# Kernel tuning notes

Hardware: AMD Instinct MI355X
Metric: run time of the kernel (lower is better)

## Reference

```python
import jax, jax.numpy as jnp
import numpy as np

H = 256      # hidden_dim
NH = 4       # num_heads
DK = H // NH # per-head dim
NL = 2       # num self-attn layers
TL = 6       # transformer_num_layers (output repeat)
PTS_DIM = 3


def _layer_norm(x, g, b, eps=1e-5):
    m = jnp.mean(x, axis=-1, keepdims=True)
    v = jnp.mean((x - m) ** 2, axis=-1, keepdims=True)
    return (x - m) / jnp.sqrt(v + eps) * g + b


def _mha(x, Wq, bq, Wk, bk, Wv, bv, Wo, bo, g, bb, bias):
    # x: [B,N,H]; bias: [B,NH,N,N]; way='add' (att_spm_type='add')
    B, N, _ = x.shape
    q = (x @ Wq + bq).reshape(B, N, NH, DK).transpose(0, 2, 1, 3)  # [B,h,N,d]
    k = (x @ Wk + bk).reshape(B, N, NH, DK).transpose(0, 2, 1, 3)
    v = (x @ Wv + bv).reshape(B, N, NH, DK).transpose(0, 2, 1, 3)
    att = jnp.einsum('bhnd,bhmd->bhnm', q, k) / np.sqrt(DK).astype(np.float32)
    att = jax.nn.softmax(att + bias, axis=-1)
    out = jnp.einsum('bhnm,bhmd->bhnd', att, v).transpose(0, 2, 1, 3).reshape(B, N, H)
    out = out @ Wo + bo
    return _layer_norm(x + out, g, bb)


def setup_inputs() -> dict:
    key = jax.random.key(0)
    ks = jax.random.split(key, 16)
    B, N = 1, 512
    s = 0.02  # weight init scale
    inp = {
        'history_states': jax.random.normal(ks[0], (TL, B, N, H), jnp.float32),
        'all_lanes_preds': jax.random.normal(ks[1], (TL, B, N, 33), jnp.float32),
        'fc_W': jax.random.normal(ks[2], (H, H), jnp.float32) * s,
        'fc_b': jnp.zeros((H,), jnp.float32),
        'Wq': jax.random.normal(ks[3], (NL, H, H), jnp.float32) * s,
        'bq': jnp.zeros((NL, H), jnp.float32),
        'Wk': jax.random.normal(ks[4], (NL, H, H), jnp.float32) * s,
        'bk': jnp.zeros((NL, H), jnp.float32),
        'Wv': jax.random.normal(ks[5], (NL, H, H), jnp.float32) * s,
        'bv': jnp.zeros((NL, H), jnp.float32),
        'Wo': jax.random.normal(ks[6], (NL, H, H), jnp.float32) * s,
        'bo': jnp.zeros((NL, H), jnp.float32),
        'ln_g': jnp.ones((NL, H), jnp.float32),
        'ln_b': jnp.zeros((NL, H), jnp.float32),
        'mlp1_W': jax.random.normal(ks[7], (H, H), jnp.float32) * s,
        'mlp1_b': jnp.zeros((H,), jnp.float32),
        'mlp2_W': jax.random.normal(ks[8], (H, H), jnp.float32) * s,
        'mlp2_b': jnp.zeros((H,), jnp.float32),
        'cls_W1': jax.random.normal(ks[9], (2 * H, H), jnp.float32) * s,
        'cls_b1': jnp.zeros((H,), jnp.float32),
        'cls_W2': jax.random.normal(ks[10], (H, 1), jnp.float32) * s,
        'cls_b2': jnp.zeros((1,), jnp.float32),
    }
    return inp


def reference(history_states, all_lanes_preds, fc_W, fc_b, Wq, bq, Wk, bk, Wv, bv,
              Wo, bo, ln_g, ln_b, mlp1_W, mlp1_b, mlp2_W, mlp2_b,
              cls_W1, cls_b1, cls_W2, cls_b2):
    query_feats = history_states[-1]                 # [B,N,H]
    coords = all_lanes_preds[-1]                      # [B,N,33]
    B, N, C = coords.shape
    coords = coords.reshape(B, N, C // PTS_DIM, PTS_DIM)
    query_end_point = coords[:, :, -1, :]             # [B,N,3]
    key_start_point = coords[:, :, 0, :]              # [B,N,3]

    # pairwise distance bias: dist[b,i,j] = ||key_start[j] - query_end[i]||
    diff = key_start_point[:, None, :, :] - query_end_point[:, :, None, :]
    dist = jnp.sqrt(jnp.sum(diff ** 2, axis=-1))[:, None, :, :]  # [B,1,N,N]
    dw = 1.0 / (dist + 0.01)
    dw = dw / jnp.sum(dw, axis=2, keepdims=True)      # normalize over dim 2
    zeros = jnp.zeros_like(dw)
    dist_weights = jax.lax.stop_gradient(
        jnp.concatenate([dw, -dist, zeros, zeros], axis=1))  # [B,4,N,N]

    # features_concat: Linear + ReLU
    x = jax.nn.relu(query_feats @ fc_W + fc_b)

    for i in range(NL):
        x = _mha(x, Wq[i], bq[i], Wk[i], bk[i], Wv[i], bv[i],
                 Wo[i], bo[i], ln_g[i], ln_b[i], dist_weights)

    # lclc relationship head: per-side MLP, pairwise concat, classifier
    o1 = jax.nn.relu(x @ mlp1_W + mlp1_b)             # [B,N,H]
    o2 = jax.nn.relu(x @ mlp2_W + mlp2_b)
    pair = jnp.concatenate([
        jnp.broadcast_to(o1[:, :, None, :], (B, N, N, H)),
        jnp.broadcast_to(o2[:, None, :, :], (B, N, N, H))], axis=-1)  # [B,N,N,2H]
    z = jax.nn.relu(pair @ cls_W1 + cls_b1)
    lclc = (z @ cls_W2 + cls_b2)[..., 0]              # [B,N,N]
    all_lclc_preds = jnp.broadcast_to(lclc[None], (TL, B, N, N))
    return all_lclc_preds
```

## Files before the change

### kernel.cpp

```cpp
#include <hip/hip_runtime.h>
#include <math.h>


#define NTOK 512
#define HDIM 256
#define DKH  64
#define NHEAD 4
#define TLEN 6
#define WSZ  65536
#define PSTR 520
#define XPS  264

typedef __attribute__((ext_vector_type(8))) short bf16x8;
typedef __attribute__((ext_vector_type(4))) float f32x4;

__device__ __forceinline__ ushort f2bf(float f)
{
    unsigned u = __builtin_bit_cast(unsigned, f);
    u += 0x7FFFu + ((u >> 16) & 1u);
    return (ushort)(u >> 16);
}

struct PKArg {
    const float* w[13];
    const float* pl;
    ushort* wpk;
    float *dist, *dwraw, *inv_cs;
};

__global__ __launch_bounds__(256) void pack_kernel(PKArg p)
{
    __shared__ __align__(16) ushort smu[64 * 72];
    const int bid = blockIdx.x;
    const int t   = threadIdx.x;

    if (bid < 208) {
        const int mat  = bid >> 4;
        const int tile = bid & 15;
        const int k0   = (tile >> 2) * 64;
        const int c0   = (tile & 3) * 64;
        const float* W = p.w[mat];
#pragma unroll
        for (int j = 0; j < 4; ++j) {
            const int i  = t + j * 256;
            const int r  = i >> 4, c4 = i & 15;
            const float4 v4 = *(const float4*)&W[(k0 + r) * HDIM + c0 + c4 * 4];
            smu[(c4 * 4 + 0) * 72 + r] = f2bf(v4.x);
            smu[(c4 * 4 + 1) * 72 + r] = f2bf(v4.y);
            smu[(c4 * 4 + 2) * 72 + r] = f2bf(v4.z);
            smu[(c4 * 4 + 3) * 72 + r] = f2bf(v4.w);
        }
        __syncthreads();
#pragma unroll
        for (int j = 0; j < 2; ++j) {
            const int i  = t + j * 256;
            const int cr = i >> 3, kk = i & 7;
            const uint4 v = *(const uint4*)&smu[cr * 72 + kk * 8];
            *(uint4*)&p.wpk[mat * WSZ + (c0 + cr) * HDIM + k0 + kk * 8] = v;
        }
    } else {
        float* smf = (float*)smu;
        float* qe  = smf;
        float* red = smf + 1536;
        const int item = bid - 208;
        for (int i = t; i < 512; i += 256) {
            qe[i * 3 + 0] = p.pl[i * 33 + 30];
            qe[i * 3 + 1] = p.pl[i * 33 + 31];
            qe[i * 3 + 2] = p.pl[i * 33 + 32];
        }
        __syncthreads();
        const int m   = item * 64 + (t & 63);
        const int nch = t >> 6;
        const float kx = p.pl[m * 33 + 0], ky = p.pl[m * 33 + 1], kz = p.pl[m * 33 + 2];
        float cs = 0.f;
        for (int n = nch * 128; n < nch * 128 + 128; ++n) {
            const float dx = kx - qe[n * 3 + 0];
            const float dy = ky - qe[n * 3 + 1];
            const float dz = kz - qe[n * 3 + 2];
            const float dd = sqrtf(dx * dx + dy * dy + dz * dz);
            const float w  = 1.0f / (dd + 0.01f);
            p.dist[n * NTOK + m]  = dd;
            p.dwraw[n * NTOK + m] = w;
            cs += w;
        }
        red[nch * 64 + (t & 63)] = cs;
        __syncthreads();
        if (t < 64)
            p.inv_cs[item * 64 + t] =
                1.0f / (red[t] + red[64 + t] + red[128 + t] + red[192 + t]);
    }
}

__device__ __forceinline__ void qkv_one(
    const ushort* __restrict__ xpan, const ushort* __restrict__ Wt,
    const float* __restrict__ bb, int p,
    int slab, int c0, int lr, int lg, int lk,
    ushort* __restrict__ q16, ushort* __restrict__ k16,
    ushort* __restrict__ vT16)
{
    const ushort* Ap = xpan + lr * XPS + lk;
    f32x4 acc[4];
#pragma unroll
    for (int j = 0; j < 4; ++j) acc[j] = (f32x4){0.f, 0.f, 0.f, 0.f};
#pragma unroll
    for (int ks = 0; ks < 8; ++ks) {
        const bf16x8 a = *(const bf16x8*)&Ap[ks * 32];
#pragma unroll
        for (int j = 0; j < 4; ++j) {
            const bf16x8 b = *(const bf16x8*)&Wt[(c0 + j * 16 + lr) * HDIM + ks * 32 + lk];
            acc[j] = __builtin_amdgcn_mfma_f32_16x16x32_bf16(a, b, acc[j], 0, 0, 0);
        }
    }
#pragma unroll
    for (int j = 0; j < 4; ++j) {
        const int col = c0 + j * 16 + lr;
        const float bv2 = bb[col];
        if (p < 2) {
            ushort* dst = (p == 0) ? q16 : k16;
#pragma unroll
            for (int rg = 0; rg < 4; ++rg)
                dst[(slab + lg * 4 + rg) * HDIM + col] = f2bf(acc[j][rg] + bv2);
        } else {
            ushort4 s = {f2bf(acc[j][0] + bv2), f2bf(acc[j][1] + bv2),
                         f2bf(acc[j][2] + bv2), f2bf(acc[j][3] + bv2)};
            *(ushort4*)&vT16[col * NTOK + slab + lg * 4] = s;
        }
    }
}

__global__ __launch_bounds__(256) void fcqkv(
    const float* __restrict__ qf, const ushort* __restrict__ fcWt,
    const float* __restrict__ fcb,
    const ushort* __restrict__ WqT, const float* __restrict__ bq,
    const ushort* __restrict__ WkT, const float* __restrict__ bk,
    const ushort* __restrict__ WvT, const float* __restrict__ bv,
    float* __restrict__ x, ushort* __restrict__ q16,
    ushort* __restrict__ k16, ushort* __restrict__ vT16)
{
    __shared__ __align__(16) ushort xpan[16 * XPS];
    const int bid  = blockIdx.x;
    const int p    = bid >> 5;
    const int slab = (bid & 31) * 16;
    const int t = threadIdx.x;
    const int wv = t >> 6, lane = t & 63;
    const int lr = lane & 15, lg = lane >> 4, lk = lg * 8;
    const int c0 = wv * 64;

    {
        f32x4 acc[4];
#pragma unroll
        for (int j = 0; j < 4; ++j) acc[j] = (f32x4){0.f, 0.f, 0.f, 0.f};
        const float* Aq = qf + (slab + lr) * HDIM + lk;
#pragma unroll
        for (int ks = 0; ks < 8; ++ks) {
            const float4 a0 = *(const float4*)&Aq[ks * 32];
            const float4 a1 = *(const float4*)&Aq[ks * 32 + 4];
            bf16x8 a;
            a[0] = (short)f2bf(a0.x); a[1] = (short)f2bf(a0.y);
            a[2] = (short)f2bf(a0.z); a[3] = (short)f2bf(a0.w);
            a[4] = (short)f2bf(a1.x); a[5] = (short)f2bf(a1.y);
            a[6] = (short)f2bf(a1.z); a[7] = (short)f2bf(a1.w);
#pragma unroll
            for (int j = 0; j < 4; ++j) {
                const bf16x8 b = *(const bf16x8*)&fcWt[(c0 + j * 16 + lr) * HDIM + ks * 32 + lk];
                acc[j] = __builtin_amdgcn_mfma_f32_16x16x32_bf16(a, b, acc[j], 0, 0, 0);
            }
        }
#pragma unroll
        for (int j = 0; j < 4; ++j) {
            const int col = c0 + j * 16 + lr;
            const float bbv = fcb[col];
#pragma unroll
            for (int rg = 0; rg < 4; ++rg) {
                const float o = fmaxf(acc[j][rg] + bbv, 0.f);
                if (p == 0) x[(slab + lg * 4 + rg) * HDIM + col] = o;
                xpan[(lg * 4 + rg) * XPS + col] = f2bf(o);
            }
        }
    }
    __syncthreads();
    const ushort* Wt = (p == 0) ? WqT : (p == 1) ? WkT : WvT;
    const float*  bb = (p == 0) ? bq  : (p == 1) ? bk  : bv;
    qkv_one(xpan, Wt, bb, p, slab, c0, lr, lg, lk, q16, k16, vT16);
}

__global__ __launch_bounds__(256) void attn_fused(
    const ushort* __restrict__ q16, const ushort* __restrict__ k16,
    const ushort* __restrict__ vT16, const float* __restrict__ dist,
    const float* __restrict__ dwraw, const float* __restrict__ inv_cs,
    ushort* __restrict__ ao16)
{
    __shared__ __align__(16) ushort P_lds[16 * PSTR];
    __shared__ __align__(16) float exch[4][16][64];
    __shared__ float rmax[4][16];
    __shared__ float psums[4][16];

    const int bid = blockIdx.x;
    const int h  = bid >> 5;
    const int n0 = (bid & 31) * 16;
    const int t  = threadIdx.x;
    const int wv = t >> 6, lane = t & 63;
    const int lr = lane & 15, lg = lane >> 4, lk = lg * 8;
    const int mW = wv * 128;

    const ushort* Qrow = q16 + (n0 + lr) * HDIM + h * DKH + lk;
    const bf16x8 a0 = *(const bf16x8*)&Qrow[0];
    const bf16x8 a1 = *(const bf16x8*)&Qrow[32];

    f32x4 accs[8];
#pragma unroll
    for (int cg = 0; cg < 8; ++cg) accs[cg] = (f32x4){0.f, 0.f, 0.f, 0.f};
#pragma unroll
    for (int cg = 0; cg < 8; ++cg) {
        const ushort* Brow = k16 + (mW + cg * 16 + lr) * HDIM + h * DKH + lk;
        accs[cg] = __builtin_amdgcn_mfma_f32_16x16x32_bf16(
            a0, *(const bf16x8*)&Brow[0], accs[cg], 0, 0, 0);
        accs[cg] = __builtin_amdgcn_mfma_f32_16x16x32_bf16(
            a1, *(const bf16x8*)&Brow[32], accs[cg], 0, 0, 0);
    }

    float s[8][4];
#pragma unroll
    for (int cg = 0; cg < 8; ++cg) {
        const int m = mW + cg * 16 + lr;
        const float ic = (h == 0) ? inv_cs[m] : 0.f;
#pragma unroll
        for (int rg = 0; rg < 4; ++rg) {
            const int n = n0 + lg * 4 + rg;
            float b = 0.f;
            if (h == 0)      b = dwraw[n * NTOK + m] * ic;
            else if (h == 1) b = -dist[n * NTOK + m];
            s[cg][rg] = accs[cg][rg] * 0.125f + b;
        }
    }

    float mx[4];
#pragma unroll
    for (int rg = 0; rg < 4; ++rg) {
        float m = s[0][rg];
#pragma unroll
        for (int cg = 1; cg < 8; ++cg) m = fmaxf(m, s[cg][rg]);
#pragma unroll
        for (int o = 1; o < 16; o <<= 1) m = fmaxf(m, __shfl_xor(m, o));
        mx[rg] = m;
    }
    if (lr == 0)
#pragma unroll
        for (int rg = 0; rg < 4; ++rg) rmax[wv][lg * 4 + rg] = mx[rg];
    __syncthreads();
    float mxf[4];
#pragma unroll
    for (int rg = 0; rg < 4; ++rg) {
        const int row = lg * 4 + rg;
        mxf[rg] = fmaxf(fmaxf(rmax[0][row], rmax[1][row]),
                        fmaxf(rmax[2][row], rmax[3][row]));
    }

    float ps[4] = {0.f, 0.f, 0.f, 0.f};
#pragma unroll
    for (int cg = 0; cg < 8; ++cg)
#pragma unroll
        for (int rg = 0; rg < 4; ++rg) {
            const float e = __expf(s[cg][rg] - mxf[rg]);
            ps[rg] += e;
            P_lds[(lg * 4 + rg) * PSTR + mW + cg * 16 + lr] = f2bf(e);
        }
#pragma unroll
    for (int rg = 0; rg < 4; ++rg) {
#pragma unroll
        for (int o = 1; o < 16; o <<= 1) ps[rg] += __shfl_xor(ps[rg], o);
    }
    if (lr == 0)
#pragma unroll
        for (int rg = 0; rg < 4; ++rg) psums[wv][lg * 4 + rg] = ps[rg];
    __syncthreads();

    f32x4 acco[4];
#pragma unroll
    for (int db = 0; db < 4; ++db) acco[db] = (f32x4){0.f, 0.f, 0.f, 0.f};
#pragma unroll
    for (int c = 0; c < 4; ++c) {
        const bf16x8 pa = *(const bf16x8*)&P_lds[lr * PSTR + mW + c * 32 + lk];
#pragma unroll
        for (int db = 0; db < 4; ++db) {
            const bf16x8 b = *(const bf16x8*)
                &vT16[(h * DKH + db * 16 + lr) * NTOK + mW + c * 32 + lk];
            acco[db] = __builtin_amdgcn_mfma_f32_16x16x32_bf16(pa, b, acco[db], 0, 0, 0);
        }
    }
#pragma unroll
    for (int db = 0; db < 4; ++db)
#pragma unroll
        for (int rg = 0; rg < 4; ++rg)
            exch[wv][lg * 4 + rg][db * 16 + lr] = acco[db][rg];
    __syncthreads();

    {
        const int r = t >> 4, d4 = t & 15;
        f32x4 sum = *(const f32x4*)&exch[0][r][d4 * 4];
        sum += *(const f32x4*)&exch[1][r][d4 * 4];
        sum += *(const f32x4*)&exch[2][r][d4 * 4];
        sum += *(const f32x4*)&exch[3][r][d4 * 4];
        const float inv = 1.0f / (psums[0][r] + psums[1][r] + psums[2][r] + psums[3][r]);
        ushort4 o = {f2bf(sum.x * inv), f2bf(sum.y * inv),
                     f2bf(sum.z * inv), f2bf(sum.w * inv)};
        *(ushort4*)&ao16[(n0 + r) * HDIM + h * DKH + d4 * 4] = o;
    }
}

__device__ __forceinline__ void oprojln_phase(
    const ushort* __restrict__ ao16, const ushort* __restrict__ WoT,
    const float* __restrict__ bo, const float* __restrict__ gamma,
    const float* __restrict__ beta, const float* __restrict__ x,
    int slab, int c0, int wv, int lr, int lg, int lk,
    float red[4][16], f32x4 acc[4])
{
    const ushort* Arow = ao16 + (slab + lr) * HDIM + lk;
#pragma unroll
    for (int j = 0; j < 4; ++j) acc[j] = (f32x4){0.f, 0.f, 0.f, 0.f};
#pragma unroll
    for (int ks = 0; ks < 8; ++ks) {
        const bf16x8 a = *(const bf16x8*)&Arow[ks * 32];
#pragma unroll
        for (int j = 0; j < 4; ++j) {
            const bf16x8 b = *(const bf16x8*)&WoT[(c0 + j * 16 + lr) * HDIM + ks * 32 + lk];
            acc[j] = __builtin_amdgcn_mfma_f32_16x16x32_bf16(a, b, acc[j], 0, 0, 0);
        }
    }
#pragma unroll
    for (int j = 0; j < 4; ++j) {
        const int col = c0 + j * 16 + lr;
        const float bc = bo[col];
#pragma unroll
        for (int rg = 0; rg < 4; ++rg)
            acc[j][rg] += bc + x[(slab + lg * 4 + rg) * HDIM + col];
    }

    float sm[4];
#pragma unroll
    for (int rg = 0; rg < 4; ++rg) {
        float s = 0.f;
#pragma unroll
        for (int j = 0; j < 4; ++j) s += acc[j][rg];
#pragma unroll
        for (int o = 1; o < 16; o <<= 1) s += __shfl_xor(s, o);
        sm[rg] = s;
    }
    if (lr == 0)
#pragma unroll
        for (int rg = 0; rg < 4; ++rg) red[wv][lg * 4 + rg] = sm[rg];
    __syncthreads();
    float mean[4];
#pragma unroll
    for (int rg = 0; rg < 4; ++rg) {
        const int row = lg * 4 + rg;
        mean[rg] = (red[0][row] + red[1][row] + red[2][row] + red[3][row]) * (1.f / 256.f);
    }
    __syncthreads();

#pragma unroll
    for (int rg = 0; rg < 4; ++rg) {
        float s2 = 0.f;
#pragma unroll
        for (int j = 0; j < 4; ++j) {
            const float c = acc[j][rg] - mean[rg];
            s2 += c * c;
        }
#pragma unroll
        for (int o = 1; o < 16; o <<= 1) s2 += __shfl_xor(s2, o);
        sm[rg] = s2;
    }
    if (lr == 0)
#pragma unroll
        for (int rg = 0; rg < 4; ++rg) red[wv][lg * 4 + rg] = sm[rg];
    __syncthreads();
    float rstd[4];
#pragma unroll
    for (int rg = 0; rg < 4; ++rg) {
        const int row = lg * 4 + rg;
        const float var = (red[0][row] + red[1][row] + red[2][row] + red[3][row]) * (1.f / 256.f);
        rstd[rg] = rsqrtf(var + 1e-5f);
    }
#pragma unroll
    for (int j = 0; j < 4; ++j) {
        const int col = c0 + j * 16 + lr;
        const float gg = gamma[col], bv = beta[col];
#pragma unroll
        for (int rg = 0; rg < 4; ++rg)
            acc[j][rg] = (acc[j][rg] - mean[rg]) * rstd[rg] * gg + bv;
    }
}

__global__ __launch_bounds__(256) void oprojqkv(
    const ushort* __restrict__ ao16, const ushort* __restrict__ WoT,
    const float* __restrict__ bo, const float* __restrict__ gamma,
    const float* __restrict__ beta,
    const ushort* __restrict__ WqT, const float* __restrict__ bq,
    const ushort* __restrict__ WkT, const float* __restrict__ bk,
    const ushort* __restrict__ WvT, const float* __restrict__ bv,
    float* __restrict__ x, ushort* __restrict__ q16,
    ushort* __restrict__ k16, ushort* __restrict__ vT16)
{
    __shared__ __align__(16) ushort xpan[16 * XPS];
    __shared__ float red[4][16];
    const int bid  = blockIdx.x;
    const int p    = bid >> 5;
    const int slab = (bid & 31) * 16;
    const int t = threadIdx.x;
    const int wv = t >> 6, lane = t & 63;
    const int lr = lane & 15, lg = lane >> 4, lk = lg * 8;
    const int c0 = wv * 64;

    f32x4 acc[4];
    oprojln_phase(ao16, WoT, bo, gamma, beta, x, slab, c0, wv, lr, lg, lk, red, acc);
#pragma unroll
    for (int j = 0; j < 4; ++j) {
        const int col = c0 + j * 16 + lr;
#pragma unroll
        for (int rg = 0; rg < 4; ++rg) {
            if (p == 0) x[(slab + lg * 4 + rg) * HDIM + col] = acc[j][rg];
            xpan[(lg * 4 + rg) * XPS + col] = f2bf(acc[j][rg]);
        }
    }
    __syncthreads();
    const ushort* Wt = (p == 0) ? WqT : (p == 1) ? WkT : WvT;
    const float*  bb = (p == 0) ? bq  : (p == 1) ? bk  : bv;
    qkv_one(xpan, Wt, bb, p, slab, c0, lr, lg, lk, q16, k16, vT16);
}

__global__ __launch_bounds__(256) void oprojmlpU(
    const ushort* __restrict__ ao16, const ushort* __restrict__ WoT,
    const float* __restrict__ bo, const float* __restrict__ gamma,
    const float* __restrict__ beta,
    const ushort* __restrict__ m1WT, const float* __restrict__ m1b,
    const ushort* __restrict__ m2WT, const float* __restrict__ m2b,
    const ushort* __restrict__ cW1aT, const float* __restrict__ cb1,
    const ushort* __restrict__ cW1bT,
    const float* __restrict__ x, float* __restrict__ U1, float* __restrict__ U2)
{
    __shared__ __align__(16) ushort xpan[16 * XPS];
    __shared__ __align__(16) ushort opan[16 * XPS];
    __shared__ float red[4][16];
    const int bid  = blockIdx.x;
    const int p    = bid >> 5;
    const int slab = (bid & 31) * 16;
    const int t = threadIdx.x;
    const int wv = t >> 6, lane = t & 63;
    const int lr = lane & 15, lg = lane >> 4, lk = lg * 8;
    const int c0 = wv * 64;

    f32x4 acc[4];
    oprojln_phase(ao16, WoT, bo, gamma, beta, x, slab, c0, wv, lr, lg, lk, red, acc);
#pragma unroll
    for (int j = 0; j < 4; ++j) {
        const int col = c0 + j * 16 + lr;
#pragma unroll
        for (int rg = 0; rg < 4; ++rg)
            xpan[(lg * 4 + rg) * XPS + col] = f2bf(acc[j][rg]);
    }
    __syncthreads();

    {
        const ushort* Wt = p ? m2WT : m1WT;
        const float*  bb = p ? m2b  : m1b;
        const ushort* Ap = xpan + lr * XPS + lk;
        f32x4 a2[4];
#pragma unroll
        for (int j = 0; j < 4; ++j) a2[j] = (f32x4){0.f, 0.f, 0.f, 0.f};
#pragma unroll
        for (int ks = 0; ks < 8; ++ks) {
            const bf16x8 a = *(const bf16x8*)&Ap[ks * 32];
#pragma unroll
            for (int j = 0; j < 4; ++j) {
                const bf16x8 b = *(const bf16x8*)&Wt[(c0 + j * 16 + lr) * HDIM + ks * 32 + lk];
                a2[j] = __builtin_amdgcn_mfma_f32_16x16x32_bf16(a, b, a2[j], 0, 0, 0);
            }
        }
#pragma unroll
        for (int j = 0; j < 4; ++j) {
            const int col = c0 + j * 16 + lr;
            const float bbv = bb[col];
#pragma unroll
            for (int rg = 0; rg < 4; ++rg)
                opan[(lg * 4 + rg) * XPS + col] = f2bf(fmaxf(a2[j][rg] + bbv, 0.f));
        }
    }
    __syncthreads();

    {
        const ushort* Wt = p ? cW1bT : cW1aT;
        float* U         = p ? U2 : U1;
        const ushort* Ao = opan + lr * XPS + lk;
        f32x4 a2[4];
#pragma unroll
        for (int j = 0; j < 4; ++j) a2[j] = (f32x4){0.f, 0.f, 0.f, 0.f};
#pragma unroll
        for (int ks = 0; ks < 8; ++ks) {
            const bf16x8 a = *(const bf16x8*)&Ao[ks * 32];
#pragma unroll
            for (int j = 0; j < 4; ++j) {
                const bf16x8 b = *(const bf16x8*)&Wt[(c0 + j * 16 + lr) * HDIM + ks * 32 + lk];
                a2[j] = __builtin_amdgcn_mfma_f32_16x16x32_bf16(a, b, a2[j], 0, 0, 0);
            }
        }
#pragma unroll
        for (int j = 0; j < 4; ++j) {
            const int col = c0 + j * 16 + lr;
            const float bbv = (p == 0) ? cb1[col] : 0.f;
#pragma unroll
            for (int rg = 0; rg < 4; ++rg)
                U[(slab + lg * 4 + rg) * HDIM + col] = a2[j][rg] + bbv;
        }
    }
}

__global__ __launch_bounds__(256) void pair_cls(const float* __restrict__ U1,
                                                const float* __restrict__ U2,
                                                const float* __restrict__ W2,
                                                const float* __restrict__ b2,
                                                float* __restrict__ out)
{
    __shared__ __align__(16) float u1s[32][260];
    __shared__ __align__(16) float u2s[32][260];
    __shared__ __align__(16) float w2s[256];
    const int t  = threadIdx.x;
    const int n0 = blockIdx.y * 32, m0 = blockIdx.x * 32;

    for (int i = t; i < 32 * 64; i += 256) {
        const int r = i >> 6, c4 = i & 63;
        *(float4*)&u1s[r][c4 * 4] = *(const float4*)&U1[(n0 + r) * HDIM + c4 * 4];
        *(float4*)&u2s[r][c4 * 4] = *(const float4*)&U2[(m0 + r) * HDIM + c4 * 4];
    }
    if (t < 64) *(float4*)&w2s[t * 4] = *(const float4*)&W2[t * 4];
    __syncthreads();

    const int tx = t & 15, ty = t >> 4;
    float acc[2][2] = {};
    for (int h4 = 0; h4 < 64; ++h4) {
        const float4 a0 = *(const float4*)&u1s[ty * 2][h4 * 4];
        const float4 a1 = *(const float4*)&u1s[ty * 2 + 1][h4 * 4];
        const float4 b0 = *(const float4*)&u2s[tx * 2][h4 * 4];
        const float4 b1 = *(const float4*)&u2s[tx * 2 + 1][h4 * 4];
        const float4 w  = *(const float4*)&w2s[h4 * 4];
#define RT(A, B) fmaxf((A) + (B), 0.f)
        acc[0][0] += RT(a0.x,b0.x)*w.x + RT(a0.y,b0.y)*w.y + RT(a0.z,b0.z)*w.z + RT(a0.w,b0.w)*w.w;
        acc[0][1] += RT(a0.x,b1.x)*w.x + RT(a0.y,b1.y)*w.y + RT(a0.z,b1.z)*w.z + RT(a0.w,b1.w)*w.w;
        acc[1][0] += RT(a1.x,b0.x)*w.x + RT(a1.y,b0.y)*w.y + RT(a1.z,b0.z)*w.z + RT(a1.w,b0.w)*w.w;
        acc[1][1] += RT(a1.x,b1.x)*w.x + RT(a1.y,b1.y)*w.y + RT(a1.z,b1.z)*w.z + RT(a1.w,b1.w)*w.w;
#undef RT
    }
    const float bbv = b2[0];
#pragma unroll
    for (int ii = 0; ii < 2; ++ii)
#pragma unroll
        for (int jj = 0; jj < 2; ++jj) {
            const float val = acc[ii][jj] + bbv;
            const int n = n0 + ty * 2 + ii;
            const int m = m0 + tx * 2 + jj;
#pragma unroll
            for (int tl = 0; tl < TLEN; ++tl)
                out[tl * NTOK * NTOK + n * NTOK + m] = val;
        }
}

extern "C" void kernel_launch(void* const* d_in, const int* in_sizes, int n_in,
                              void* d_out, int out_size, void* d_ws, size_t ws_size,
                              hipStream_t stream)
{
    const float* hs   = (const float*)d_in[0];
    const float* qf   = hs + 5 * NTOK * HDIM;
    const float* alp  = (const float*)d_in[1];
    const float* pl   = alp + 5 * NTOK * 33;
    const float* fc_W = (const float*)d_in[2];
    const float* fc_b = (const float*)d_in[3];
    const float* Wq   = (const float*)d_in[4];
    const float* bq   = (const float*)d_in[5];
    const float* Wk   = (const float*)d_in[6];
    const float* bk   = (const float*)d_in[7];
    const float* Wv   = (const float*)d_in[8];
    const float* bv   = (const float*)d_in[9];
    const float* Wo   = (const float*)d_in[10];
    const float* bo   = (const float*)d_in[11];
    const float* lng  = (const float*)d_in[12];
    const float* lnb  = (const float*)d_in[13];
    const float* m1W  = (const float*)d_in[14];
    const float* m1b  = (const float*)d_in[15];
    const float* m2W  = (const float*)d_in[16];
    const float* m2b  = (const float*)d_in[17];
    const float* cW1  = (const float*)d_in[18];
    const float* cb1  = (const float*)d_in[19];
    const float* cW2  = (const float*)d_in[20];
    const float* cb2  = (const float*)d_in[21];
    float* out = (float*)d_out;

    const int NN  = NTOK * NTOK;
    const int NH_ = NTOK * HDIM;
    float* ws     = (float*)d_ws;
    float* dist   = ws;
    float* dwraw  = ws + NN;
    float* inv_cs = ws + 2 * NN;
    float* x      = ws + 2 * NN + 512;
    float* U1     = x + NH_;
    float* U2     = U1 + NH_;
    ushort* u16   = (ushort*)(U2 + NH_);
    ushort* wpk   = u16;
    ushort* q16   = wpk + 13 * WSZ;
    ushort* k16   = q16 + NH_;
    ushort* vT16  = k16 + NH_;
    ushort* ao16  = vT16 + NH_;

    PKArg pk;
    pk.w[0]  = fc_W;
    pk.w[1]  = Wq;  pk.w[2]  = Wq + WSZ;
    pk.w[3]  = Wk;  pk.w[4]  = Wk + WSZ;
    pk.w[5]  = Wv;  pk.w[6]  = Wv + WSZ;
    pk.w[7]  = Wo;  pk.w[8]  = Wo + WSZ;
    pk.w[9]  = m1W; pk.w[10] = m2W;
    pk.w[11] = cW1; pk.w[12] = cW1 + WSZ;
    pk.pl = pl;
    pk.wpk = wpk;
    pk.dist = dist; pk.dwraw = dwraw; pk.inv_cs = inv_cs;
    pack_kernel<<<216, 256, 0, stream>>>(pk);

    fcqkv<<<96, 256, 0, stream>>>(
        qf, wpk + 0 * WSZ, fc_b,
        wpk + 1 * WSZ, bq, wpk + 3 * WSZ, bk, wpk + 5 * WSZ, bv,
        x, q16, k16, vT16);

    attn_fused<<<128, 256, 0, stream>>>(q16, k16, vT16, dist, dwraw, inv_cs, ao16);

    oprojqkv<<<96, 256, 0, stream>>>(
        ao16, wpk + 7 * WSZ, bo, lng, lnb,
        wpk + 2 * WSZ, bq + HDIM, wpk + 4 * WSZ, bk + HDIM,
        wpk + 6 * WSZ, bv + HDIM,
        x, q16, k16, vT16);

    attn_fused<<<128, 256, 0, stream>>>(q16, k16, vT16, dist, dwraw, inv_cs, ao16);

    oprojmlpU<<<64, 256, 0, stream>>>(
        ao16, wpk + 8 * WSZ, bo + HDIM, lng + HDIM, lnb + HDIM,
        wpk + 9 * WSZ, m1b, wpk + 10 * WSZ, m2b,
        wpk + 11 * WSZ, cb1, wpk + 12 * WSZ,
        x, U1, U2);

    pair_cls<<<dim3(16, 16), 256, 0, stream>>>(U1, U2, cW2, cb2, out);
}
```

Before: 110.9 us.

## Split QKV/MLP output columns across twice the blocks and widen attention to 8 waves

The fused fc+QKV, oproj+QKV and oproj+MLP kernels now launch twice as many blocks. Each block computes half the output columns (128 instead of 256) for its projection, and the preceding fc or oproj/LN phase is recomputed redundantly in each half. Attention blocks use 512 threads, with 8 waves each covering 64 keys, and the cross-wave reduction is widened to match. The residual x is double-buffered (xa/xb) so recomputing blocks do not race with the write of the updated x. The goal is better CU occupancy on the small 512-token problem, paid for with duplicated prologue GEMMs and larger reductions.

Measured after the change: 97.69 us. -11.9%, faster.

```diff
diff --git a/kernel.cpp b/kernel.cpp
--- a/kernel.cpp
+++ b/kernel.cpp
@@ -91,32 +91,32 @@
     }
 }
 
-__device__ __forceinline__ void qkv_one(
+__device__ __forceinline__ void qkv_one2(
     const ushort* __restrict__ xpan, const ushort* __restrict__ Wt,
-    const float* __restrict__ bb, int p,
+    const float* __restrict__ bb, int prob,
     int slab, int c0, int lr, int lg, int lk,
     ushort* __restrict__ q16, ushort* __restrict__ k16,
     ushort* __restrict__ vT16)
 {
     const ushort* Ap = xpan + lr * XPS + lk;
-    f32x4 acc[4];
-#pragma unroll
-    for (int j = 0; j < 4; ++j) acc[j] = (f32x4){0.f, 0.f, 0.f, 0.f};
+    f32x4 acc[2];
+    acc[0] = (f32x4){0.f, 0.f, 0.f, 0.f};
+    acc[1] = (f32x4){0.f, 0.f, 0.f, 0.f};
 #pragma unroll
     for (int ks = 0; ks < 8; ++ks) {
         const bf16x8 a = *(const bf16x8*)&Ap[ks * 32];
 #pragma unroll
-        for (int j = 0; j < 4; ++j) {
+        for (int j = 0; j < 2; ++j) {
             const bf16x8 b = *(const bf16x8*)&Wt[(c0 + j * 16 + lr) * HDIM + ks * 32 + lk];
             acc[j] = __builtin_amdgcn_mfma_f32_16x16x32_bf16(a, b, acc[j], 0, 0, 0);
         }
     }
 #pragma unroll
-    for (int j = 0; j < 4; ++j) {
+    for (int j = 0; j < 2; ++j) {
         const int col = c0 + j * 16 + lr;
         const float bv2 = bb[col];
-        if (p < 2) {
-            ushort* dst = (p == 0) ? q16 : k16;
+        if (prob < 2) {
+            ushort* dst = (prob == 0) ? q16 : k16;
 #pragma unroll
             for (int rg = 0; rg < 4; ++rg)
                 dst[(slab + lg * 4 + rg) * HDIM + col] = f2bf(acc[j][rg] + bv2);
@@ -134,12 +134,12 @@
     const ushort* __restrict__ WqT, const float* __restrict__ bq,
     const ushort* __restrict__ WkT, const float* __restrict__ bk,
     const ushort* __restrict__ WvT, const float* __restrict__ bv,
-    float* __restrict__ x, ushort* __restrict__ q16,
+    float* __restrict__ xa, ushort* __restrict__ q16,
     ushort* __restrict__ k16, ushort* __restrict__ vT16)
 {
     __shared__ __align__(16) ushort xpan[16 * XPS];
     const int bid  = blockIdx.x;
-    const int p    = bid >> 5;
+    const int p6   = bid >> 5;
     const int slab = (bid & 31) * 16;
     const int t = threadIdx.x;
     const int wv = t >> 6, lane = t & 63;
@@ -173,27 +173,29 @@
 #pragma unroll
             for (int rg = 0; rg < 4; ++rg) {
                 const float o = fmaxf(acc[j][rg] + bbv, 0.f);
-                if (p == 0) x[(slab + lg * 4 + rg) * HDIM + col] = o;
+                if (p6 == 0) xa[(slab + lg * 4 + rg) * HDIM + col] = o;
                 xpan[(lg * 4 + rg) * XPS + col] = f2bf(o);
             }
         }
     }
     __syncthreads();
-    const ushort* Wt = (p == 0) ? WqT : (p == 1) ? WkT : WvT;
-    const float*  bb = (p == 0) ? bq  : (p == 1) ? bk  : bv;
-    qkv_one(xpan, Wt, bb, p, slab, c0, lr, lg, lk, q16, k16, vT16);
-}
-
-__global__ __launch_bounds__(256) void attn_fused(
+    const int prob = p6 >> 1, ch = p6 & 1;
+    const ushort* Wt = (prob == 0) ? WqT : (prob == 1) ? WkT : WvT;
+    const float*  bb = (prob == 0) ? bq  : (prob == 1) ? bk  : bv;
+    qkv_one2(xpan, Wt, bb, prob, slab, ch * 128 + wv * 32, lr, lg, lk,
+             q16, k16, vT16);
+}
+
+__global__ __launch_bounds__(512) void attn_fused(
     const ushort* __restrict__ q16, const ushort* __restrict__ k16,
     const ushort* __restrict__ vT16, const float* __restrict__ dist,
     const float* __restrict__ dwraw, const float* __restrict__ inv_cs,
     ushort* __restrict__ ao16)
 {
     __shared__ __align__(16) ushort P_lds[16 * PSTR];
-    __shared__ __align__(16) float exch[4][16][64];
-    __shared__ float rmax[4][16];
-    __shared__ float psums[4][16];
+    __shared__ __align__(16) float exch[8][16][64];
+    __shared__ float rmax[8][16];
+    __shared__ float psums[8][16];
 
     const int bid = blockIdx.x;
     const int h  = bid >> 5;
@@ -201,17 +203,17 @@
     const int t  = threadIdx.x;
     const int wv = t >> 6, lane = t & 63;
     const int lr = lane & 15, lg = lane >> 4, lk = lg * 8;
-    const int mW = wv * 128;
+    const int mW = wv * 64;
 
     const ushort* Qrow = q16 + (n0 + lr) * HDIM + h * DKH + lk;
     const bf16x8 a0 = *(const bf16x8*)&Qrow[0];
     const bf16x8 a1 = *(const bf16x8*)&Qrow[32];
 
-    f32x4 accs[8];
-#pragma unroll
-    for (int cg = 0; cg < 8; ++cg) accs[cg] = (f32x4){0.f, 0.f, 0.f, 0.f};
-#pragma unroll
-    for (int cg = 0; cg < 8; ++cg) {
+    f32x4 accs[4];
+#pragma unroll
+    for (int cg = 0; cg < 4; ++cg) accs[cg] = (f32x4){0.f, 0.f, 0.f, 0.f};
+#pragma unroll
+    for (int cg = 0; cg < 4; ++cg) {
         const ushort* Brow = k16 + (mW + cg * 16 + lr) * HDIM + h * DKH + lk;
         accs[cg] = __builtin_amdgcn_mfma_f32_16x16x32_bf16(
             a0, *(const bf16x8*)&Brow[0], accs[cg], 0, 0, 0);
@@ -219,9 +221,9 @@
             a1, *(const bf16x8*)&Brow[32], accs[cg], 0, 0, 0);
     }
 
-    float s[8][4];
-#pragma unroll
-    for (int cg = 0; cg < 8; ++cg) {
+    float s[4][4];
+#pragma unroll
+    for (int cg = 0; cg < 4; ++cg) {
         const int m = mW + cg * 16 + lr;
         const float ic = (h == 0) ? inv_cs[m] : 0.f;
 #pragma unroll
@@ -237,9 +239,7 @@
     float mx[4];
 #pragma unroll
     for (int rg = 0; rg < 4; ++rg) {
-        float m = s[0][rg];
-#pragma unroll
-        for (int cg = 1; cg < 8; ++cg) m = fmaxf(m, s[cg][rg]);
+        float m = fmaxf(fmaxf(s[0][rg], s[1][rg]), fmaxf(s[2][rg], s[3][rg]));
 #pragma unroll
         for (int o = 1; o < 16; o <<= 1) m = fmaxf(m, __shfl_xor(m, o));
         mx[rg] = m;
@@ -252,13 +252,15 @@
 #pragma unroll
     for (int rg = 0; rg < 4; ++rg) {
         const int row = lg * 4 + rg;
-        mxf[rg] = fmaxf(fmaxf(rmax[0][row], rmax[1][row]),
-                        fmaxf(rmax[2][row], rmax[3][row]));
+        float m = rmax[0][row];
+#pragma unroll
+        for (int w = 1; w < 8; ++w) m = fmaxf(m, rmax[w][row]);
+        mxf[rg] = m;
     }
 
     float ps[4] = {0.f, 0.f, 0.f, 0.f};
 #pragma unroll
-    for (int cg = 0; cg < 8; ++cg)
+    for (int cg = 0; cg < 4; ++cg)
 #pragma unroll
         for (int rg = 0; rg < 4; ++rg) {
             const float e = __expf(s[cg][rg] - mxf[rg]);
@@ -279,7 +281,7 @@
 #pragma unroll
     for (int db = 0; db < 4; ++db) acco[db] = (f32x4){0.f, 0.f, 0.f, 0.f};
 #pragma unroll
-    for (int c = 0; c < 4; ++c) {
+    for (int c = 0; c < 2; ++c) {
         const bf16x8 pa = *(const bf16x8*)&P_lds[lr * PSTR + mW + c * 32 + lk];
 #pragma unroll
         for (int db = 0; db < 4; ++db) {
@@ -296,15 +298,17 @@
     __syncthreads();
 
     {
-        const int r = t >> 4, d4 = t & 15;
-        f32x4 sum = *(const f32x4*)&exch[0][r][d4 * 4];
-        sum += *(const f32x4*)&exch[1][r][d4 * 4];
-        sum += *(const f32x4*)&exch[2][r][d4 * 4];
-        sum += *(const f32x4*)&exch[3][r][d4 * 4];
-        const float inv = 1.0f / (psums[0][r] + psums[1][r] + psums[2][r] + psums[3][r]);
-        ushort4 o = {f2bf(sum.x * inv), f2bf(sum.y * inv),
-                     f2bf(sum.z * inv), f2bf(sum.w * inv)};
-        *(ushort4*)&ao16[(n0 + r) * HDIM + h * DKH + d4 * 4] = o;
+        const int r = t >> 5, dp = (t & 31) * 2;
+        float sx = 0.f, sy = 0.f, den = 0.f;
+#pragma unroll
+        for (int w = 0; w < 8; ++w) {
+            const float2 e = *(const float2*)&exch[w][r][dp];
+            sx += e.x; sy += e.y;
+            den += psums[w][r];
+        }
+        const float inv = 1.0f / den;
+        ushort2 o = {f2bf(sx * inv), f2bf(sy * inv)};
+        *(ushort2*)&ao16[(n0 + r) * HDIM + h * DKH + dp] = o;
     }
 }
 
@@ -398,13 +402,14 @@
     const ushort* __restrict__ WqT, const float* __restrict__ bq,
     const ushort* __restrict__ WkT, const float* __restrict__ bk,
     const ushort* __restrict__ WvT, const float* __restrict__ bv,
-    float* __restrict__ x, ushort* __restrict__ q16,
-    ushort* __restrict__ k16, ushort* __restrict__ vT16)
+    const float* __restrict__ xa, float* __restrict__ xb,
+    ushort* __restrict__ q16, ushort* __restrict__ k16,
+    ushort* __restrict__ vT16)
 {
     __shared__ __align__(16) ushort xpan[16 * XPS];
     __shared__ float red[4][16];
     const int bid  = blockIdx.x;
-    const int p    = bid >> 5;
+    const int p6   = bid >> 5;
     const int slab = (bid & 31) * 16;
     const int t = threadIdx.x;
     const int wv = t >> 6, lane = t & 63;
@@ -412,20 +417,22 @@
     const int c0 = wv * 64;
 
     f32x4 acc[4];
-    oprojln_phase(ao16, WoT, bo, gamma, beta, x, slab, c0, wv, lr, lg, lk, red, acc);
+    oprojln_phase(ao16, WoT, bo, gamma, beta, xa, slab, c0, wv, lr, lg, lk, red, acc);
 #pragma unroll
     for (int j = 0; j < 4; ++j) {
         const int col = c0 + j * 16 + lr;
 #pragma unroll
         for (int rg = 0; rg < 4; ++rg) {
-            if (p == 0) x[(slab + lg * 4 + rg) * HDIM + col] = acc[j][rg];
+            if (p6 == 0) xb[(slab + lg * 4 + rg) * HDIM + col] = acc[j][rg];
             xpan[(lg * 4 + rg) * XPS + col] = f2bf(acc[j][rg]);
         }
     }
     __syncthreads();
-    const ushort* Wt = (p == 0) ? WqT : (p == 1) ? WkT : WvT;
-    const float*  bb = (p == 0) ? bq  : (p == 1) ? bk  : bv;
-    qkv_one(xpan, Wt, bb, p, slab, c0, lr, lg, lk, q16, k16, vT16);
+    const int prob = p6 >> 1, ch = p6 & 1;
+    const ushort* Wt = (prob == 0) ? WqT : (prob == 1) ? WkT : WvT;
+    const float*  bb = (prob == 0) ? bq  : (prob == 1) ? bk  : bv;
+    qkv_one2(xpan, Wt, bb, prob, slab, ch * 128 + wv * 32, lr, lg, lk,
+             q16, k16, vT16);
 }
 
 __global__ __launch_bounds__(256) void oprojmlpU(
@@ -436,13 +443,14 @@
     const ushort* __restrict__ m2WT, const float* __restrict__ m2b,
     const ushort* __restrict__ cW1aT, const float* __restrict__ cb1,
     const ushort* __restrict__ cW1bT,
-    const float* __restrict__ x, float* __restrict__ U1, float* __restrict__ U2)
+    const float* __restrict__ xb, float* __restrict__ U1, float* __restrict__ U2)
 {
     __shared__ __align__(16) ushort xpan[16 * XPS];
     __shared__ __align__(16) ushort opan[16 * XPS];
     __shared__ float red[4][16];
     const int bid  = blockIdx.x;
-    const int p    = bid >> 5;
+    const int p4   = bid >> 5;
+    const int p    = p4 >> 1, ch = p4 & 1;
     const int slab = (bid & 31) * 16;
     const int t = threadIdx.x;
     const int wv = t >> 6, lane = t & 63;
@@ -450,7 +458,7 @@
     const int c0 = wv * 64;
 
     f32x4 acc[4];
-    oprojln_phase(ao16, WoT, bo, gamma, beta, x, slab, c0, wv, lr, lg, lk, red, acc);
+    oprojln_phase(ao16, WoT, bo, gamma, beta, xb, slab, c0, wv, lr, lg, lk, red, acc);
 #pragma unroll
     for (int j = 0; j < 4; ++j) {
         const int col = c0 + j * 16 + lr;
@@ -490,22 +498,23 @@
     {
         const ushort* Wt = p ? cW1bT : cW1aT;
         float* U         = p ? U2 : U1;
+        const int cb     = ch * 128 + wv * 32;
         const ushort* Ao = opan + lr * XPS + lk;
-        f32x4 a2[4];
-#pragma unroll
-        for (int j = 0; j < 4; ++j) a2[j] = (f32x4){0.f, 0.f, 0.f, 0.f};
+        f32x4 a2[2];
+        a2[0] = (f32x4){0.f, 0.f, 0.f, 0.f};
+        a2[1] = (f32x4){0.f, 0.f, 0.f, 0.f};
 #pragma unroll
         for (int ks = 0; ks < 8; ++ks) {
             const bf16x8 a = *(const bf16x8*)&Ao[ks * 32];
 #pragma unroll
-            for (int j = 0; j < 4; ++j) {
-                const bf16x8 b = *(const bf16x8*)&Wt[(c0 + j * 16 + lr) * HDIM + ks * 32 + lk];
+            for (int j = 0; j < 2; ++j) {
+                const bf16x8 b = *(const bf16x8*)&Wt[(cb + j * 16 + lr) * HDIM + ks * 32 + lk];
                 a2[j] = __builtin_amdgcn_mfma_f32_16x16x32_bf16(a, b, a2[j], 0, 0, 0);
             }
         }
 #pragma unroll
-        for (int j = 0; j < 4; ++j) {
-            const int col = c0 + j * 16 + lr;
+        for (int j = 0; j < 2; ++j) {
+            const int col = cb + j * 16 + lr;
             const float bbv = (p == 0) ? cb1[col] : 0.f;
 #pragma unroll
             for (int rg = 0; rg < 4; ++rg)
@@ -599,8 +608,9 @@
     float* dist   = ws;
     float* dwraw  = ws + NN;
     float* inv_cs = ws + 2 * NN;
-    float* x      = ws + 2 * NN + 512;
-    float* U1     = x + NH_;
+    float* xa     = ws + 2 * NN + 512;
+    float* xb     = xa + NH_;
+    float* U1     = xb + NH_;
     float* U2     = U1 + NH_;
     ushort* u16   = (ushort*)(U2 + NH_);
     ushort* wpk   = u16;
@@ -622,26 +632,26 @@
     pk.dist = dist; pk.dwraw = dwraw; pk.inv_cs = inv_cs;
     pack_kernel<<<216, 256, 0, stream>>>(pk);
 
-    fcqkv<<<96, 256, 0, stream>>>(
+    fcqkv<<<192, 256, 0, stream>>>(
         qf, wpk + 0 * WSZ, fc_b,
         wpk + 1 * WSZ, bq, wpk + 3 * WSZ, bk, wpk + 5 * WSZ, bv,
-        x, q16, k16, vT16);
-
-    attn_fused<<<128, 256, 0, stream>>>(q16, k16, vT16, dist, dwraw, inv_cs, ao16);
-
-    oprojqkv<<<96, 256, 0, stream>>>(
+        xa, q16, k16, vT16);
+
+    attn_fused<<<128, 512, 0, stream>>>(q16, k16, vT16, dist, dwraw, inv_cs, ao16);
+
+    oprojqkv<<<192, 256, 0, stream>>>(
         ao16, wpk + 7 * WSZ, bo, lng, lnb,
         wpk + 2 * WSZ, bq + HDIM, wpk + 4 * WSZ, bk + HDIM,
         wpk + 6 * WSZ, bv + HDIM,
-        x, q16, k16, vT16);
-
-    attn_fused<<<128, 256, 0, stream>>>(q16, k16, vT16, dist, dwraw, inv_cs, ao16);
-
-    oprojmlpU<<<64, 256, 0, stream>>>(
+        xa, xb, q16, k16, vT16);
+
+    attn_fused<<<128, 512, 0, stream>>>(q16, k16, vT16, dist, dwraw, inv_cs, ao16);
+
+    oprojmlpU<<<128, 256, 0, stream>>>(
         ao16, wpk + 8 * WSZ, bo + HDIM, lng + HDIM, lnb + HDIM,
         wpk + 9 * WSZ, m1b, wpk + 10 * WSZ, m2b,
         wpk + 11 * WSZ, cb1, wpk + 12 * WSZ,
-        x, U1, U2);
+        xb, U1, U2);
 
     pair_cls<<<dim3(16, 16), 256, 0, stream>>>(U1, U2, cW2, cb2, out);
 }
```
